# Kernel tuning notes

Measured on AMD Instinct MI355X. Metric: run time of the kernel, lower is better.

Reference implementation:

```python
import jax, jax.numpy as jnp
import numpy as np

NUM_HEADS = 14
SCALE = 0.125  # fixed constant in the source, not 1/sqrt(head_dim)
PATCH = 14
DIM = 3 * PATCH * PATCH  # 588


def setup_inputs() -> dict:
    key = jax.random.key(0)
    k_x, k_cw, k_cb, k_qw, k_qb = jax.random.split(key, 5)
    B, C_in, H, W = 8, 3, 448, 448
    x = jax.random.normal(k_x, (B, C_in, H, W), dtype=jnp.float32)
    # Conv2d(in_channels=3, dim, kernel=patch, stride=patch), torch layout OIHW
    fan_in = C_in * PATCH * PATCH
    bound = 1.0 / np.sqrt(fan_in)
    conv_w = jax.random.uniform(k_cw, (DIM, C_in, PATCH, PATCH), jnp.float32, -bound, bound)
    conv_b = jax.random.uniform(k_cb, (DIM,), jnp.float32, -bound, bound)
    # Linear(dim, 3*dim): weight [out, in] torch layout
    lb = 1.0 / np.sqrt(DIM)
    qkv_w = jax.random.uniform(k_qw, (3 * DIM, DIM), jnp.float32, -lb, lb)
    qkv_b = jax.random.uniform(k_qb, (3 * DIM,), jnp.float32, -lb, lb)
    return {"x": x, "conv_w": conv_w, "conv_b": conv_b, "qkv_w": qkv_w, "qkv_b": qkv_b}


def reference(x, conv_w, conv_b, qkv_w, qkv_b):
    # Patch embedding: conv kernel==stride==patch  -> [B, DIM, H/p, W/p]
    y = jax.lax.conv_general_dilated(
        x, conv_w, window_strides=(PATCH, PATCH), padding="VALID",
        dimension_numbers=("NCHW", "OIHW", "NCHW"))
    y = y + conv_b[None, :, None, None]
    B = y.shape[0]
    # flatten(2).transpose(1, 2) -> [B, N, C]
    tokens = y.reshape(B, DIM, -1).transpose(0, 2, 1)
    N, C = tokens.shape[1], tokens.shape[2]
    hd = C // NUM_HEADS  # 42
    qkv = tokens @ qkv_w.T + qkv_b  # [B, N, 3C]
    qkv = qkv.reshape(B, N, 3, NUM_HEADS, hd).transpose(2, 0, 3, 1, 4)  # [3,B,H,N,hd]
    q, k, v = qkv[0], qkv[1], qkv[2]
    attn = jnp.einsum("bhnd,bhmd->bhnm", q, k) * SCALE  # [B,H,N,N]
    attn = jax.nn.softmax(attn, axis=-1)
    out = jnp.einsum("bhnm,bhmd->bhnd", attn, v)  # [B,H,N,hd]
    out = out.transpose(0, 2, 1, 3).reshape(B, N, C)  # [B,N,C]
    return out
```

## Files before the change

kernel.cpp:

```cpp
#include <hip/hip_runtime.h>

typedef unsigned short u16;
typedef __attribute__((ext_vector_type(8))) short bf16x8;
typedef __attribute__((ext_vector_type(4))) float f32x4;

#define MTOK 8192
#define KP   640
#define CC   588
#define C3   1764
#define NH   14
#define SEQ  1024
#define HD   42
#define DP   64
#define DV   48

static __device__ __forceinline__ u16 f2b(float f) {
  unsigned u = __builtin_bit_cast(unsigned, f);
  u = (u + 0x7FFFu + ((u >> 16) & 1u)) >> 16;
  return (u16)u;
}

static __device__ __forceinline__ void gl_lds16(const void* g, void* l) {
  auto gp = (const unsigned int __attribute__((address_space(1)))*)((unsigned long long)g);
  auto lp = (unsigned int __attribute__((address_space(3)))*)((unsigned long long)l);
  __builtin_amdgcn_global_load_lds(gp, lp, 16, 0, 0);
}

__global__ void im2col_k(const float* __restrict__ x, u16* __restrict__ A) {
  int t = blockIdx.x;
  int b = t >> 10, pi = t & 1023, ph = pi >> 5, pw = pi & 31;
  const float* xb = x + (size_t)b * 3 * 448 * 448;
  for (int kk = threadIdx.x; kk < KP; kk += 256) {
    float v = 0.f;
    if (kk < CC) {
      int c = kk / 196, rem = kk - c * 196, i = rem / 14, j = rem - i * 14;
      v = xb[(size_t)(c * 448 + ph * 14 + i) * 448 + pw * 14 + j];
    }
    A[(size_t)t * KP + kk] = f2b(v);
  }
}

__global__ void padw_k(const float* __restrict__ w, u16* __restrict__ dst, int R) {
  int r = blockIdx.x;
  for (int c = threadIdx.x; c < KP; c += 256) {
    float v = (r < R && c < CC) ? w[(size_t)r * CC + c] : 0.f;
    dst[(size_t)r * KP + c] = f2b(v);
  }
}

template <int MODE>
__global__ void __launch_bounds__(256, 2) gemm_k(
    const u16* __restrict__ A, const u16* __restrict__ Bt,
    const float* __restrict__ bias, u16* __restrict__ out0,
    u16* __restrict__ qb, u16* __restrict__ kb, u16* __restrict__ vb) {
  __shared__ alignas(16) u16 sA[128 * 64];
  __shared__ alignas(16) u16 sB[128 * 64];
  const int tid = threadIdx.x;
  const int wave = tid >> 6, lane = tid & 63, quad = lane >> 4, l16 = lane & 15;
  const int wi = wave >> 1, wj = wave & 1;
  const int m0 = blockIdx.x * 128, n0 = blockIdx.y * 128;
  const int rL = lane >> 3, scid = lane & 7;
  const f32x4 z4 = {0.f, 0.f, 0.f, 0.f};

  f32x4 acc[4][4];
#pragma unroll
  for (int i = 0; i < 4; i++)
#pragma unroll
    for (int j = 0; j < 4; j++) acc[i][j] = z4;

  for (int k0 = 0; k0 < KP; k0 += 64) {
    __syncthreads();
#pragma unroll
    for (int cc = wave; cc < 16; cc += 4) {
      int r = cc * 8 + rL;
      int sch = scid ^ (r & 7);
      gl_lds16(A + ((size_t)(m0 + r) * KP + k0 + sch * 8), &sA[cc * 512]);
    }
#pragma unroll
    for (int cc = wave; cc < 16; cc += 4) {
      int r = cc * 8 + rL;
      int sch = scid ^ (r & 7);
      gl_lds16(Bt + ((size_t)(n0 + r) * KP + k0 + sch * 8), &sB[cc * 512]);
    }
    __syncthreads();
#pragma unroll
    for (int ks = 0; ks < 2; ks++) {
      bf16x8 af[4], bfr[4];
#pragma unroll
      for (int i = 0; i < 4; i++) {
        int r = wi * 64 + i * 16 + l16;
        int ch = (ks * 4 + quad) ^ (r & 7);
        af[i] = *(const bf16x8*)&sA[r * 64 + ch * 8];
      }
#pragma unroll
      for (int j = 0; j < 4; j++) {
        int r = wj * 64 + j * 16 + l16;
        int ch = (ks * 4 + quad) ^ (r & 7);
        bfr[j] = *(const bf16x8*)&sB[r * 64 + ch * 8];
      }
#pragma unroll
      for (int i = 0; i < 4; i++)
#pragma unroll
        for (int j = 0; j < 4; j++)
          acc[i][j] = __builtin_amdgcn_mfma_f32_16x16x32_bf16(af[i], bfr[j], acc[i][j], 0, 0, 0);
    }
  }

  const int baser = wi * 64 + quad * 4;
  if (MODE == 0) {
#pragma unroll
    for (int j = 0; j < 4; j++) {
      int col = n0 + wj * 64 + j * 16 + l16;
      float bs = (col < CC) ? bias[col] : 0.f;
#pragma unroll
      for (int i = 0; i < 4; i++) {
        int row = m0 + baser + i * 16;
#pragma unroll
        for (int r = 0; r < 4; r++)
          out0[(size_t)(row + r) * KP + col] = f2b(acc[i][j][r] + bs);
      }
    }
  } else {
#pragma unroll
    for (int j = 0; j < 4; j++) {
      int col = n0 + wj * 64 + j * 16 + l16;
      if (col < C3) {
        float bs = bias[col];
        int which = col / CC;
        int rem = col - which * CC;
        int h = rem / HD;
        int d = rem - h * HD;
        u16* dst = (which == 0) ? qb : (which == 1) ? kb : vb;
#pragma unroll
        for (int i = 0; i < 4; i++) {
          int row = m0 + baser + i * 16;
#pragma unroll
          for (int r = 0; r < 4; r++) {
            int rw = row + r;
            int b = rw >> 10, n = rw & 1023;
            dst[((size_t)((b * NH + h) * SEQ + n)) * DP + d] = f2b(acc[i][j][r] + bs);
          }
        }
      }
    }
  }
}

__global__ void vtrans_k(const u16* __restrict__ vb, u16* __restrict__ vT) {
  __shared__ u16 tile[64 * 49];
  int bh = blockIdx.x, mt = blockIdx.y;
  for (int idx = threadIdx.x; idx < 64 * DV; idx += 256) {
    int n = idx / DV, d = idx - n * DV;
    u16 v = 0;
    if (d < HD) v = vb[((size_t)(bh * SEQ + mt * 64 + n)) * DP + d];
    tile[n * 49 + d] = v;
  }
  __syncthreads();
  for (int idx = threadIdx.x; idx < DV * 64; idx += 256) {
    int d = idx >> 6, n = idx & 63;
    u16 v = (d < HD) ? tile[n * 49 + d] : ((d == HD) ? (u16)0x3F80 : (u16)0);
    vT[((size_t)(bh * DV + d)) * SEQ + mt * 64 + n] = v;
  }
}

__global__ void __launch_bounds__(256, 2) attn_k(
    const u16* __restrict__ qb, const u16* __restrict__ kb,
    const u16* __restrict__ vT, float* __restrict__ out) {
  __shared__ alignas(16) u16 sK[64 * 64];
  __shared__ alignas(16) u16 sV[DV * 64];
  __shared__ alignas(16) u16 sP[256 * 72];
  __shared__ float lbuf[256];
  const int tid = threadIdx.x;
  const int wave = tid >> 6, lane = tid & 63, quad = lane >> 4, l16 = lane & 15;
  const int g = blockIdx.x;
  const int bh = (g & 7) * 14 + (g >> 5);
  const int qt = (g >> 3) & 3;
  const int q0 = qt * 256;
  const int rL = lane >> 3, scid = lane & 7;
  const float SC2 = 0.18033688011112042f;
  const f32x4 z4 = {0.f, 0.f, 0.f, 0.f};
  const int prow = wave * 64;

  bf16x8 aq[4][2];
#pragma unroll
  for (int i = 0; i < 4; i++) {
    const u16* qrow = qb + ((size_t)(bh * SEQ + q0 + wave * 64 + i * 16 + l16)) * DP;
    aq[i][0] = *(const bf16x8*)&qrow[quad * 8];
    aq[i][1] = *(const bf16x8*)&qrow[32 + quad * 8];
  }
  f32x4 o[4][3];
#pragma unroll
  for (int i = 0; i < 4; i++)
#pragma unroll
    for (int j = 0; j < 3; j++) o[i][j] = z4;
  const u16* kb0 = kb + (size_t)bh * SEQ * DP;
  const u16* vb0 = vT + (size_t)bh * DV * SEQ;

  for (int kt = 0; kt < 16; kt++) {
    const int m0 = kt * 64;
    __syncthreads();
    {
      const u16* ktile = kb0 + (size_t)m0 * DP;
#pragma unroll
      for (int cc = wave; cc < 8; cc += 4) {
        int r = cc * 8 + rL;
        gl_lds16(ktile + ((size_t)r * 64 + (scid ^ (r & 7)) * 8), &sK[cc * 512]);
      }
#pragma unroll
      for (int cc = wave; cc < 6; cc += 4) {
        int d = cc * 8 + rL;
        gl_lds16(vb0 + ((size_t)d * SEQ + m0 + (scid ^ (d & 7)) * 8), &sV[cc * 512]);
      }
    }
    __syncthreads();
    bf16x8 bk[4][2];
#pragma unroll
    for (int j = 0; j < 4; j++) {
      int n = j * 16 + l16;
#pragma unroll
      for (int ks = 0; ks < 2; ks++)
        bk[j][ks] = *(const bf16x8*)&sK[n * 64 + (((ks * 4 + quad) ^ (n & 7)) * 8)];
    }
#pragma unroll
    for (int i = 0; i < 4; i++) {
#pragma unroll
      for (int j = 0; j < 4; j++) {
        f32x4 s = z4;
        s = __builtin_amdgcn_mfma_f32_16x16x32_bf16(aq[i][0], bk[j][0], s, 0, 0, 0);
        s = __builtin_amdgcn_mfma_f32_16x16x32_bf16(aq[i][1], bk[j][1], s, 0, 0, 0);
#pragma unroll
        for (int r = 0; r < 4; r++)
          sP[(prow + i * 16 + quad * 4 + r) * 72 + j * 16 + l16] =
              f2b(__builtin_amdgcn_exp2f(s[r] * SC2));
      }
    }
#pragma unroll
    for (int ks = 0; ks < 2; ks++) {
      bf16x8 bv[3];
#pragma unroll
      for (int j = 0; j < 3; j++) {
        int d = j * 16 + l16;
        bv[j] = *(const bf16x8*)&sV[d * 64 + (((ks * 4 + quad) ^ (d & 7)) * 8)];
      }
#pragma unroll
      for (int i = 0; i < 4; i++) {
        bf16x8 ap = *(const bf16x8*)&sP[(prow + i * 16 + l16) * 72 + ks * 32 + quad * 8];
#pragma unroll
        for (int j = 0; j < 3; j++)
          o[i][j] = __builtin_amdgcn_mfma_f32_16x16x32_bf16(ap, bv[j], o[i][j], 0, 0, 0);
      }
    }
  }
  __syncthreads();
  if (l16 == 10) {
#pragma unroll
    for (int i = 0; i < 4; i++)
#pragma unroll
      for (int r = 0; r < 4; r++)
        lbuf[prow + i * 16 + quad * 4 + r] = o[i][2][r];
  }
  __syncthreads();
  const int b = bh / NH, h = bh - b * NH;
#pragma unroll
  for (int i = 0; i < 4; i++) {
#pragma unroll
    for (int r = 0; r < 4; r++) {
      int row = prow + i * 16 + quad * 4 + r;
      float rc = 1.f / lbuf[row];
      float* orow = out + ((size_t)(b * SEQ + q0 + row)) * CC + h * HD;
#pragma unroll
      for (int j = 0; j < 3; j++) {
        int d = j * 16 + l16;
        if (d < HD) orow[d] = o[i][j][r] * rc;
      }
    }
  }
}

extern "C" void kernel_launch(void* const* d_in, const int* in_sizes, int n_in,
                              void* d_out, int out_size, void* d_ws, size_t ws_size,
                              hipStream_t stream) {
  (void)in_sizes; (void)n_in; (void)out_size; (void)ws_size;
  const float* x      = (const float*)d_in[0];
  const float* conv_w = (const float*)d_in[1];
  const float* conv_b = (const float*)d_in[2];
  const float* qkv_w  = (const float*)d_in[3];
  const float* qkv_b  = (const float*)d_in[4];
  float* out = (float*)d_out;

  char* ws = (char*)d_ws;
  size_t off = 0;
  u16* A      = (u16*)(ws + off); off += (size_t)MTOK * KP * 2;
  u16* Wc     = (u16*)(ws + off); off += (size_t)640 * KP * 2;
  u16* Wq     = (u16*)(ws + off); off += (size_t)1792 * KP * 2;
  u16* tokens = (u16*)(ws + off); off += (size_t)MTOK * KP * 2;
  u16* qbuf   = (u16*)(ws + off); off += (size_t)112 * SEQ * DP * 2;
  u16* kbuf   = (u16*)(ws + off); off += (size_t)112 * SEQ * DP * 2;
  u16* vbuf   = (u16*)(ws + off); off += (size_t)112 * SEQ * DP * 2;
  u16* vTb    = (u16*)(ws + off); off += (size_t)112 * DV * SEQ * 2;

  hipMemsetAsync(kbuf, 0, (size_t)112 * SEQ * DP * 2, stream);
  im2col_k<<<MTOK, 256, 0, stream>>>(x, A);
  padw_k<<<640, 256, 0, stream>>>(conv_w, Wc, CC);
  padw_k<<<1792, 256, 0, stream>>>(qkv_w, Wq, C3);
  gemm_k<0><<<dim3(64, 5), 256, 0, stream>>>(A, Wc, conv_b, tokens, nullptr, nullptr, nullptr);
  gemm_k<1><<<dim3(64, 14), 256, 0, stream>>>(tokens, Wq, qkv_b, nullptr, qbuf, kbuf, vbuf);
  vtrans_k<<<dim3(112, 16), 256, 0, stream>>>(vbuf, vTb);
  attn_k<<<448, 256, 0, stream>>>(qbuf, kbuf, vTb, out);
}
```

Measured before the change: 193.4 us.

## Load K/V fragments directly to registers with prefetch, drop block-wide syncs in attention

The attention kernel no longer stages K and V tiles through shared memory with block barriers. Each wave now loads its K and V MFMA fragments straight from global memory into registers, prefetching the next tile while computing the current one, and keeps a private P buffer so no __syncthreads is needed. K rows are permuted (4*l16+j) so that P can be written as packed bf16 pairs with a cheaper round-to-nearest pack. The softmax scale is folded into Q in the QKV GEMM epilogue, and the row-sum is fetched with a shuffle instead of an LDS buffer. The risks are more register pressure from the dropped occupancy hint, and redundant global loads of K/V by every wave.

```diff
diff --git a/kernel.cpp b/kernel.cpp
--- a/kernel.cpp
+++ b/kernel.cpp
@@ -1,6 +1,7 @@
 #include <hip/hip_runtime.h>
 
 typedef unsigned short u16;
+typedef unsigned int u32;
 typedef __attribute__((ext_vector_type(8))) short bf16x8;
 typedef __attribute__((ext_vector_type(4))) float f32x4;
 
@@ -13,6 +14,7 @@
 #define HD   42
 #define DP   64
 #define DV   48
+#define SC2f 0.18033688011112042f
 
 static __device__ __forceinline__ u16 f2b(float f) {
   unsigned u = __builtin_bit_cast(unsigned, f);
@@ -24,6 +26,12 @@
   auto gp = (const unsigned int __attribute__((address_space(1)))*)((unsigned long long)g);
   auto lp = (unsigned int __attribute__((address_space(3)))*)((unsigned long long)l);
   __builtin_amdgcn_global_load_lds(gp, lp, 16, 0, 0);
+}
+
+static __device__ __forceinline__ u32 pk2(float lo, float hi) {
+  u32 a = __builtin_bit_cast(u32, lo) + 0x8000u;
+  u32 b = __builtin_bit_cast(u32, hi) + 0x8000u;
+  return __builtin_amdgcn_perm(b, a, 0x07060302u);
 }
 
 __global__ void im2col_k(const float* __restrict__ x, u16* __restrict__ A) {
@@ -73,14 +81,12 @@
 #pragma unroll
     for (int cc = wave; cc < 16; cc += 4) {
       int r = cc * 8 + rL;
-      int sch = scid ^ (r & 7);
-      gl_lds16(A + ((size_t)(m0 + r) * KP + k0 + sch * 8), &sA[cc * 512]);
+      gl_lds16(A + ((size_t)(m0 + r) * KP + k0 + (scid ^ (r & 7)) * 8), &sA[cc * 512]);
     }
 #pragma unroll
     for (int cc = wave; cc < 16; cc += 4) {
       int r = cc * 8 + rL;
-      int sch = scid ^ (r & 7);
-      gl_lds16(Bt + ((size_t)(n0 + r) * KP + k0 + sch * 8), &sB[cc * 512]);
+      gl_lds16(Bt + ((size_t)(n0 + r) * KP + k0 + (scid ^ (r & 7)) * 8), &sB[cc * 512]);
     }
     __syncthreads();
 #pragma unroll
@@ -89,14 +95,12 @@
 #pragma unroll
       for (int i = 0; i < 4; i++) {
         int r = wi * 64 + i * 16 + l16;
-        int ch = (ks * 4 + quad) ^ (r & 7);
-        af[i] = *(const bf16x8*)&sA[r * 64 + ch * 8];
+        af[i] = *(const bf16x8*)&sA[r * 64 + (((ks * 4 + quad) ^ (r & 7)) * 8)];
       }
 #pragma unroll
       for (int j = 0; j < 4; j++) {
         int r = wj * 64 + j * 16 + l16;
-        int ch = (ks * 4 + quad) ^ (r & 7);
-        bfr[j] = *(const bf16x8*)&sB[r * 64 + ch * 8];
+        bfr[j] = *(const bf16x8*)&sB[r * 64 + (((ks * 4 + quad) ^ (r & 7)) * 8)];
       }
 #pragma unroll
       for (int i = 0; i < 4; i++)
@@ -131,6 +135,7 @@
         int h = rem / HD;
         int d = rem - h * HD;
         u16* dst = (which == 0) ? qb : (which == 1) ? kb : vb;
+        float sc = (which == 0) ? SC2f : 1.0f;
 #pragma unroll
         for (int i = 0; i < 4; i++) {
           int row = m0 + baser + i * 16;
@@ -138,7 +143,7 @@
           for (int r = 0; r < 4; r++) {
             int rw = row + r;
             int b = rw >> 10, n = rw & 1023;
-            dst[((size_t)((b * NH + h) * SEQ + n)) * DP + d] = f2b(acc[i][j][r] + bs);
+            dst[((size_t)((b * NH + h) * SEQ + n)) * DP + d] = f2b((acc[i][j][r] + bs) * sc);
           }
         }
       }
@@ -163,23 +168,18 @@
   }
 }
 
-__global__ void __launch_bounds__(256, 2) attn_k(
+__global__ void __launch_bounds__(256) attn_k(
     const u16* __restrict__ qb, const u16* __restrict__ kb,
     const u16* __restrict__ vT, float* __restrict__ out) {
-  __shared__ alignas(16) u16 sK[64 * 64];
-  __shared__ alignas(16) u16 sV[DV * 64];
-  __shared__ alignas(16) u16 sP[256 * 72];
-  __shared__ float lbuf[256];
+  __shared__ alignas(16) u16 sP[4][64 * 72];
   const int tid = threadIdx.x;
   const int wave = tid >> 6, lane = tid & 63, quad = lane >> 4, l16 = lane & 15;
   const int g = blockIdx.x;
   const int bh = (g & 7) * 14 + (g >> 5);
   const int qt = (g >> 3) & 3;
   const int q0 = qt * 256;
-  const int rL = lane >> 3, scid = lane & 7;
-  const float SC2 = 0.18033688011112042f;
   const f32x4 z4 = {0.f, 0.f, 0.f, 0.f};
-  const int prow = wave * 64;
+  u16* sPw = sP[wave];
 
   bf16x8 aq[4][2];
 #pragma unroll
@@ -193,80 +193,70 @@
   for (int i = 0; i < 4; i++)
 #pragma unroll
     for (int j = 0; j < 3; j++) o[i][j] = z4;
+
   const u16* kb0 = kb + (size_t)bh * SEQ * DP;
   const u16* vb0 = vT + (size_t)bh * DV * SEQ;
 
+  bf16x8 bk[4][2];
+  bf16x8 bv[2][3];
+#define LOADK(m0_)                                                                       \
+  {                                                                                      \
+    _Pragma("unroll") for (int j = 0; j < 4; j++) {                                      \
+      const u16* kr = kb0 + ((size_t)((m0_) + 4 * l16 + j)) * DP + quad * 8;             \
+      bk[j][0] = *(const bf16x8*)kr;                                                     \
+      bk[j][1] = *(const bf16x8*)(kr + 32);                                              \
+    }                                                                                    \
+  }
+#define LOADV(m0_)                                                                       \
+  {                                                                                      \
+    _Pragma("unroll") for (int ks = 0; ks < 2; ks++)                                     \
+    _Pragma("unroll") for (int j = 0; j < 3; j++)                                        \
+      bv[ks][j] = *(const bf16x8*)(vb0 + (size_t)(j * 16 + l16) * SEQ + (m0_) + ks * 32 + quad * 8); \
+  }
+  LOADK(0);
+  LOADV(0);
+
   for (int kt = 0; kt < 16; kt++) {
-    const int m0 = kt * 64;
-    __syncthreads();
-    {
-      const u16* ktile = kb0 + (size_t)m0 * DP;
-#pragma unroll
-      for (int cc = wave; cc < 8; cc += 4) {
-        int r = cc * 8 + rL;
-        gl_lds16(ktile + ((size_t)r * 64 + (scid ^ (r & 7)) * 8), &sK[cc * 512]);
-      }
-#pragma unroll
-      for (int cc = wave; cc < 6; cc += 4) {
-        int d = cc * 8 + rL;
-        gl_lds16(vb0 + ((size_t)d * SEQ + m0 + (scid ^ (d & 7)) * 8), &sV[cc * 512]);
-      }
-    }
-    __syncthreads();
-    bf16x8 bk[4][2];
-#pragma unroll
-    for (int j = 0; j < 4; j++) {
-      int n = j * 16 + l16;
-#pragma unroll
-      for (int ks = 0; ks < 2; ks++)
-        bk[j][ks] = *(const bf16x8*)&sK[n * 64 + (((ks * 4 + quad) ^ (n & 7)) * 8)];
-    }
+    const int m1 = ((kt + 1) & 15) * 64;
 #pragma unroll
     for (int i = 0; i < 4; i++) {
+      f32x4 s[4];
 #pragma unroll
       for (int j = 0; j < 4; j++) {
-        f32x4 s = z4;
-        s = __builtin_amdgcn_mfma_f32_16x16x32_bf16(aq[i][0], bk[j][0], s, 0, 0, 0);
-        s = __builtin_amdgcn_mfma_f32_16x16x32_bf16(aq[i][1], bk[j][1], s, 0, 0, 0);
-#pragma unroll
-        for (int r = 0; r < 4; r++)
-          sP[(prow + i * 16 + quad * 4 + r) * 72 + j * 16 + l16] =
-              f2b(__builtin_amdgcn_exp2f(s[r] * SC2));
-      }
-    }
+        f32x4 t = __builtin_amdgcn_mfma_f32_16x16x32_bf16(aq[i][0], bk[j][0], z4, 0, 0, 0);
+        s[j] = __builtin_amdgcn_mfma_f32_16x16x32_bf16(aq[i][1], bk[j][1], t, 0, 0, 0);
+      }
+#pragma unroll
+      for (int r = 0; r < 4; r++) {
+        u32 d0 = pk2(__builtin_amdgcn_exp2f(s[0][r]), __builtin_amdgcn_exp2f(s[1][r]));
+        u32 d1 = pk2(__builtin_amdgcn_exp2f(s[2][r]), __builtin_amdgcn_exp2f(s[3][r]));
+        u32* dst = (u32*)&sPw[(i * 16 + quad * 4 + r) * 72 + l16 * 4];
+        dst[0] = d0;
+        dst[1] = d1;
+      }
+    }
+    LOADK(m1);
 #pragma unroll
     for (int ks = 0; ks < 2; ks++) {
-      bf16x8 bv[3];
-#pragma unroll
-      for (int j = 0; j < 3; j++) {
-        int d = j * 16 + l16;
-        bv[j] = *(const bf16x8*)&sV[d * 64 + (((ks * 4 + quad) ^ (d & 7)) * 8)];
-      }
 #pragma unroll
       for (int i = 0; i < 4; i++) {
-        bf16x8 ap = *(const bf16x8*)&sP[(prow + i * 16 + l16) * 72 + ks * 32 + quad * 8];
+        bf16x8 ap = *(const bf16x8*)&sPw[(i * 16 + l16) * 72 + ks * 32 + quad * 8];
 #pragma unroll
         for (int j = 0; j < 3; j++)
-          o[i][j] = __builtin_amdgcn_mfma_f32_16x16x32_bf16(ap, bv[j], o[i][j], 0, 0, 0);
-      }
-    }
-  }
-  __syncthreads();
-  if (l16 == 10) {
-#pragma unroll
-    for (int i = 0; i < 4; i++)
-#pragma unroll
-      for (int r = 0; r < 4; r++)
-        lbuf[prow + i * 16 + quad * 4 + r] = o[i][2][r];
-  }
-  __syncthreads();
+          o[i][j] = __builtin_amdgcn_mfma_f32_16x16x32_bf16(ap, bv[ks][j], o[i][j], 0, 0, 0);
+      }
+    }
+    LOADV(m1);
+  }
+
   const int b = bh / NH, h = bh - b * NH;
 #pragma unroll
   for (int i = 0; i < 4; i++) {
 #pragma unroll
     for (int r = 0; r < 4; r++) {
-      int row = prow + i * 16 + quad * 4 + r;
-      float rc = 1.f / lbuf[row];
+      float ls = __shfl(o[i][2][r], (lane & 48) + 10, 64);
+      float rc = 1.f / ls;
+      int row = wave * 64 + i * 16 + quad * 4 + r;
       float* orow = out + ((size_t)(b * SEQ + q0 + row)) * CC + h * HD;
 #pragma unroll
       for (int j = 0; j < 3; j++) {
@@ -275,6 +265,8 @@
       }
     }
   }
+#undef LOADK
+#undef LOADV
 }
 
 extern "C" void kernel_launch(void* const* d_in, const int* in_sizes, int n_in,
```

Result: slower. 205.7 us (+6.4%).
